# Performance work log

Hardware: AMD Instinct MI355X
Metric: run time of the kernel (lower is better)

The kernel has to match this reference:

```python
import jax, jax.numpy as jnp
import numpy as np

D_K = 64

def setup_inputs() -> dict:
    key = jax.random.key(0)
    kx, kq, kk, kv = jax.random.split(key, 4)
    B, T, D = 4, 2048, 1024
    s = 1.0 / np.sqrt(D)
    return {
        "x": jax.random.normal(kx, (B, T, D), dtype=jnp.float32),
        "Wq": jax.random.normal(kq, (D, D_K), dtype=jnp.float32) * s,
        "Wk": jax.random.normal(kk, (D, D_K), dtype=jnp.float32) * s,
        "Wv": jax.random.normal(kv, (D, D_K), dtype=jnp.float32) * s,
    }

def reference(x, Wq, Wk, Wv):
    # x: [B, T, D]; Wq/Wk/Wv: [D, d_k]
    Q = x @ Wq  # [B, T, d_k]
    K = x @ Wk
    V = x @ Wv
    scale = 1.0 / jnp.sqrt(jnp.asarray(Q.shape[-1], Q.dtype))
    scores = jnp.einsum('btd,bsd->bts', Q, K) * scale  # [B, T, T]
    T = scores.shape[-1]
    causal = jnp.tril(jnp.ones((T, T), dtype=bool))  # keep lower-tri incl diag
    masked = jnp.where(causal, scores, -jnp.inf)
    attn = jax.nn.softmax(masked, axis=-1)  # dropout p=0.0 -> identity
    context = jnp.einsum('bts,bsd->btd', attn, V)  # [B, T, d_k]
    return context
```

## Files before the change

### kernel.cpp

```cpp
#include <hip/hip_runtime.h>
#include <math.h>

#define BT    8192
#define TSEQ  2048
#define DIN   1024
#define DK    64

typedef __attribute__((ext_vector_type(8))) short bf16x8;
typedef __attribute__((ext_vector_type(4))) short bf16x4;
typedef __attribute__((ext_vector_type(4))) float f32x4;

static __device__ inline unsigned short f2bf(float f) {
    union { float f; unsigned u; } v; v.f = f;
    unsigned r = v.u + 0x7fff + ((v.u >> 16) & 1);
    return (unsigned short)(r >> 16);
}

static __device__ inline bf16x4 cvt4(float4 a) {
    bf16x4 r;
    r[0] = (short)f2bf(a.x); r[1] = (short)f2bf(a.y);
    r[2] = (short)f2bf(a.z); r[3] = (short)f2bf(a.w);
    return r;
}

__global__ __launch_bounds__(256) void wt_kernel(
    const float* __restrict__ Wq, const float* __restrict__ Wk,
    const float* __restrict__ Wv, unsigned short* __restrict__ WT)
{
    __shared__ float ws[64][65];
    const int tid = threadIdx.x;
    const int mat = blockIdx.x >> 4;
    const int k0  = (blockIdx.x & 15) << 6;
    const float* W = (mat == 0) ? Wq : ((mat == 1) ? Wk : Wv);

    const int j = tid & 63;
    for (int i = tid >> 6; i < 64; i += 4)
        ws[i][j] = W[(size_t)(k0 + i) * DK + j];
    __syncthreads();

    const int n  = tid & 63;
    const int c0 = (tid >> 6) << 4;
    unsigned short* dst = WT + (size_t)(mat * 64 + n) * DIN + k0 + c0;
    #pragma unroll
    for (int c = 0; c < 16; ++c) dst[c] = f2bf(ws[c0 + c][n]);
}

__global__ __launch_bounds__(256, 2) void proj_kernel(
    const float* __restrict__ x, const unsigned short* __restrict__ WT,
    unsigned short* __restrict__ Qb, unsigned short* __restrict__ Kb,
    unsigned short* __restrict__ VT)
{
    __shared__ unsigned short xs[16][1032];
    __shared__ unsigned short wtb[192][72];
    const int tid = threadIdx.x;
    const int m0 = blockIdx.x * 16;

    {
        const int r = tid >> 4;
        const int c = (tid & 15) << 2;
        const float* src = x + (size_t)(m0 + r) * DIN + c;
        float4 tmp[16];
        #pragma unroll
        for (int s = 0; s < 16; ++s) tmp[s] = *(const float4*)(src + s * 64);
        #pragma unroll
        for (int s = 0; s < 16; ++s) *(bf16x4*)&xs[r][c + s * 64] = cvt4(tmp[s]);
    }

    const int lane = tid & 63;
    const int w    = tid >> 6;
    const int lr = lane & 15, lg = lane >> 4;

    f32x4 acc[3];
    #pragma unroll
    for (int nt = 0; nt < 3; ++nt) acc[nt] = (f32x4){0.f, 0.f, 0.f, 0.f};

    const unsigned short* wt_w = WT + (size_t)w * 48 * DIN;
    bf16x8 cur[6], nxt[6];
    #pragma unroll
    for (int i = 0; i < 6; ++i) {
        const int c = lane + i * 64;
        const int nl = c >> 3;
        const int sl = c & 7;
        cur[i] = *(const bf16x8*)(wt_w + (size_t)nl * DIN + (sl << 3));
    }

    __syncthreads();

    for (int kc = 0; kc < 16; ++kc) {
        const int k0 = kc << 6;

        if (kc + 1 < 16) {
            #pragma unroll
            for (int i = 0; i < 6; ++i) {
                const int c = lane + i * 64;
                const int nl = c >> 3;
                const int sl = c & 7;
                nxt[i] = *(const bf16x8*)(wt_w + (size_t)nl * DIN
                                          + (k0 + 64) + (sl << 3));
            }
        }

        #pragma unroll
        for (int i = 0; i < 6; ++i) {
            const int c = lane + i * 64;
            const int n = w * 48 + (c >> 3);
            const int sl = c & 7;
            *(bf16x8*)&wtb[n][((sl + n) & 7) << 3] = cur[i];
        }
        asm volatile("s_waitcnt lgkmcnt(0)" ::: "memory");

        #pragma unroll
        for (int st = 0; st < 2; ++st) {
            const bf16x8 af = *(const bf16x8*)&xs[lr][k0 + (st << 5) + (lg << 3)];
            #pragma unroll
            for (int nt = 0; nt < 3; ++nt) {
                const int n = w * 48 + nt * 16 + lr;
                const int sl = (st << 2) + lg;
                const bf16x8 bf = *(const bf16x8*)&wtb[n][((sl + n) & 7) << 3];
                acc[nt] = __builtin_amdgcn_mfma_f32_16x16x32_bf16(af, bf, acc[nt], 0, 0, 0);
            }
        }

        if (kc + 1 < 16) {
            #pragma unroll
            for (int i = 0; i < 6; ++i) cur[i] = nxt[i];
        }
    }

    const float qsc = 0.125f * 1.44269504088896340736f;
    #pragma unroll
    for (int nt = 0; nt < 3; ++nt) {
        const int gct = w * 3 + nt;
        if (gct < 8) {
            #pragma unroll
            for (int r = 0; r < 4; ++r) {
                const int row = m0 + (lg << 2) + r;
                const float vv = acc[nt][r];
                if (gct < 4) Qb[(size_t)row * DK + gct * 16 + lr] = f2bf(vv * qsc);
                else         Kb[(size_t)row * DK + (gct - 4) * 16 + lr] = f2bf(vv);
            }
        } else {
            const int d = (gct - 8) * 16 + lr;
            const int t = m0 + (lg << 2);
            const int tb = t & (TSEQ - 1);
            const size_t tile = (size_t)(t >> 11) * 32 + (tb >> 6);
            ushort4 pk;
            pk.x = f2bf(acc[nt][0]); pk.y = f2bf(acc[nt][1]);
            pk.z = f2bf(acc[nt][2]); pk.w = f2bf(acc[nt][3]);
            *(ushort4*)&VT[(tile * DK + d) * 64 + (tb & 63)] = pk;
        }
    }
}

__global__ __launch_bounds__(256, 2) void attn_kernel(
    const unsigned short* __restrict__ Qb, const unsigned short* __restrict__ Kb,
    const unsigned short* __restrict__ VT, float* __restrict__ O)
{
    __shared__ __align__(16) unsigned short P_lds[4][16][72];
    __shared__ float Opart[4][16][68];
    __shared__ float mpart[4][16];
    __shared__ float Lpart[4][16];

    const int lane = threadIdx.x & 63;
    const int w    = threadIdx.x >> 6;
    const int i    = blockIdx.x;
    const int half = i >> 8;
    const int k    = i & 255;
    const int batch = k & 3;
    const int j    = k >> 2;
    const int qt_local = half ? j : (127 - j);
    const int q0 = (batch << 11) + (qt_local << 4);
    const int t0 = qt_local << 4;
    const int b  = batch;
    const int lr = lane & 15;
    const int lg = lane >> 4;

    const unsigned short* Qrow = Qb + (size_t)(q0 + lr) * DK + (lg << 3);
    const bf16x8 qf0 = *(const bf16x8*)(Qrow);
    const bf16x8 qf1 = *(const bf16x8*)(Qrow + 32);

    const unsigned short* Kbase = Kb + (size_t)b * TSEQ * DK;
    const unsigned short* Vbase = VT + (size_t)b * 32 * DK * 64;

    f32x4 oacc[4];
    #pragma unroll
    for (int dt = 0; dt < 4; ++dt) oacc[dt] = (f32x4){0.f, 0.f, 0.f, 0.f};
    float m[4] = {-INFINITY, -INFINITY, -INFINITY, -INFINITY};
    float L[4] = {0.f, 0.f, 0.f, 0.f};

    const int nkb = (t0 >> 6) + 1;

    bf16x8 kf0[4], kf1[4];
    if (w < nkb) {
        const int s0 = w << 6;
        #pragma unroll
        for (int ct = 0; ct < 4; ++ct) {
            const unsigned short* Krow =
                Kbase + (size_t)(s0 + ct * 16 + lr) * DK + (lg << 3);
            kf0[ct] = *(const bf16x8*)(Krow);
            kf1[ct] = *(const bf16x8*)(Krow + 32);
        }
    }

    for (int kb = w; kb < nkb; kb += 4) {
        const int s0 = kb << 6;

        f32x4 s[4];
        #pragma unroll
        for (int ct = 0; ct < 4; ++ct) {
            f32x4 a = (f32x4){0.f, 0.f, 0.f, 0.f};
            a = __builtin_amdgcn_mfma_f32_16x16x32_bf16(qf0, kf0[ct], a, 0, 0, 0);
            a = __builtin_amdgcn_mfma_f32_16x16x32_bf16(qf1, kf1[ct], a, 0, 0, 0);
            s[ct] = a;
        }

        bf16x8 vf0[4], vf1[4];
        {
            const unsigned short* Vtile = Vbase + (size_t)kb * DK * 64;
            #pragma unroll
            for (int dt = 0; dt < 4; ++dt) {
                const unsigned short* Vrow = Vtile + (dt * 16 + lr) * 64 + (lg << 3);
                vf0[dt] = *(const bf16x8*)(Vrow);
                vf1[dt] = *(const bf16x8*)(Vrow + 32);
            }
        }

        bf16x8 nk0[4], nk1[4];
        if (kb + 4 < nkb) {
            const int sn = (kb + 4) << 6;
            #pragma unroll
            for (int ct = 0; ct < 4; ++ct) {
                const unsigned short* Krow =
                    Kbase + (size_t)(sn + ct * 16 + lr) * DK + (lg << 3);
                nk0[ct] = *(const bf16x8*)(Krow);
                nk1[ct] = *(const bf16x8*)(Krow + 32);
            }
        }

        if (kb == nkb - 1) {
            #pragma unroll
            for (int ct = 0; ct < 4; ++ct)
                #pragma unroll
                for (int r = 0; r < 4; ++r)
                    if (s0 + ct * 16 + lr > t0 + lg * 4 + r) s[ct][r] = -INFINITY;
        }

        float pm[4];
        #pragma unroll
        for (int r = 0; r < 4; ++r)
            pm[r] = fmaxf(fmaxf(s[0][r], s[1][r]), fmaxf(s[2][r], s[3][r]));

        bool near = true;
        #pragma unroll
        for (int r = 0; r < 4; ++r)
            near = near && (pm[r] - m[r] <= 8.0f);

        if (!__all(near)) {
            float tmax[4];
            #pragma unroll
            for (int r = 0; r < 4; ++r) tmax[r] = pm[r];
            #pragma unroll
            for (int off = 1; off < 16; off <<= 1)
                #pragma unroll
                for (int r = 0; r < 4; ++r)
                    tmax[r] = fmaxf(tmax[r], __shfl_xor(tmax[r], off));

            float f[4];
            #pragma unroll
            for (int r = 0; r < 4; ++r) {
                const float mn = fmaxf(m[r], tmax[r]);
                f[r] = exp2f(m[r] - mn);
                m[r] = mn;
            }
            #pragma unroll
            for (int r = 0; r < 4; ++r) L[r] *= f[r];
            #pragma unroll
            for (int r = 0; r < 4; ++r) {
                oacc[0][r] *= f[r]; oacc[1][r] *= f[r];
                oacc[2][r] *= f[r]; oacc[3][r] *= f[r];
            }
        }

        float ps[4] = {0.f, 0.f, 0.f, 0.f};
        unsigned short pb[4][4];
        #pragma unroll
        for (int ct = 0; ct < 4; ++ct)
            #pragma unroll
            for (int r = 0; r < 4; ++r) {
                const float p = exp2f(s[ct][r] - m[r]);
                ps[r] += p;
                pb[ct][r] = f2bf(p);
            }
        #pragma unroll
        for (int r = 0; r < 4; ++r) L[r] += ps[r];

        #pragma unroll
        for (int ct = 0; ct < 4; ++ct)
            #pragma unroll
            for (int r = 0; r < 4; ++r)
                P_lds[w][lg * 4 + r][ct * 16 + lr] = pb[ct][r];
        asm volatile("s_waitcnt lgkmcnt(0)" ::: "memory");
        const bf16x8 pf0 = *(const bf16x8*)&P_lds[w][lr][(lg << 3)];
        const bf16x8 pf1 = *(const bf16x8*)&P_lds[w][lr][32 + (lg << 3)];

        #pragma unroll
        for (int dt = 0; dt < 4; ++dt) {
            oacc[dt] = __builtin_amdgcn_mfma_f32_16x16x32_bf16(pf0, vf0[dt], oacc[dt], 0, 0, 0);
            oacc[dt] = __builtin_amdgcn_mfma_f32_16x16x32_bf16(pf1, vf1[dt], oacc[dt], 0, 0, 0);
        }

        #pragma unroll
        for (int ct = 0; ct < 4; ++ct) { kf0[ct] = nk0[ct]; kf1[ct] = nk1[ct]; }
    }

    #pragma unroll
    for (int off = 1; off < 16; off <<= 1)
        #pragma unroll
        for (int r = 0; r < 4; ++r) L[r] += __shfl_xor(L[r], off);

    #pragma unroll
    for (int dt = 0; dt < 4; ++dt)
        #pragma unroll
        for (int r = 0; r < 4; ++r)
            Opart[w][(lg << 2) + r][dt * 16 + lr] = oacc[dt][r];
    if (lr == 0) {
        #pragma unroll
        for (int r = 0; r < 4; ++r) {
            mpart[w][(lg << 2) + r] = m[r];
            Lpart[w][(lg << 2) + r] = L[r];
        }
    }
    __syncthreads();

    #pragma unroll
    for (int r = 0; r < 4; ++r) {
        const int row = (lg << 2) + r;
        const float M = fmaxf(fmaxf(mpart[0][row], mpart[1][row]),
                              fmaxf(mpart[2][row], mpart[3][row]));
        float Lf = 0.f, o = 0.f;
        #pragma unroll
        for (int v = 0; v < 4; ++v) {
            const float fv = exp2f(mpart[v][row] - M);
            Lf += fv * Lpart[v][row];
            o  += fv * Opart[v][row][(w << 4) + lr];
        }
        O[(size_t)(q0 + row) * DK + (w << 4) + lr] = o / Lf;
    }
}

extern "C" void kernel_launch(void* const* d_in, const int* in_sizes, int n_in,
                              void* d_out, int out_size, void* d_ws, size_t ws_size,
                              hipStream_t stream) {
    const float* x  = (const float*)d_in[0];
    const float* Wq = (const float*)d_in[1];
    const float* Wk = (const float*)d_in[2];
    const float* Wv = (const float*)d_in[3];
    float* O = (float*)d_out;

    unsigned short* Qb = (unsigned short*)d_ws;
    unsigned short* Kb = Qb + (size_t)BT * DK;
    unsigned short* VT = Kb + (size_t)BT * DK;
    unsigned short* WT = VT + (size_t)BT * DK;

    wt_kernel  <<<dim3(48),  dim3(256), 0, stream>>>(Wq, Wk, Wv, WT);
    proj_kernel<<<dim3(512), dim3(256), 0, stream>>>(x, WT, Qb, Kb, VT);
    attn_kernel<<<dim3(512), dim3(256), 0, stream>>>(Qb, Kb, VT, O);
}
```

Before: 42.08 us.

## Process two query tiles per block with eight waves sharing K/V loads

The attention kernel now handles two adjacent 16-row query tiles per block. Each K/V tile loaded from global memory feeds the MFMAs for both query tiles, and eight waves split the key range instead of four. The grid drops to 256 blocks of 512 threads, and the software prefetch of the next K tile is removed. The cost is higher register pressure, a larger two-pass LDS reduction with an extra barrier, fewer blocks to balance the causal workload, and loss of K-load latency hiding.

```diff
diff --git a/kernel.cpp b/kernel.cpp
--- a/kernel.cpp
+++ b/kernel.cpp
@@ -152,47 +152,54 @@
     }
 }
 
-__global__ __launch_bounds__(256, 2) void attn_kernel(
+__global__ __launch_bounds__(512, 2) void attn_kernel(
     const unsigned short* __restrict__ Qb, const unsigned short* __restrict__ Kb,
     const unsigned short* __restrict__ VT, float* __restrict__ O)
 {
-    __shared__ __align__(16) unsigned short P_lds[4][16][72];
-    __shared__ float Opart[4][16][68];
-    __shared__ float mpart[4][16];
-    __shared__ float Lpart[4][16];
+    __shared__ __align__(16) unsigned short P_lds[8][16][72];
+    __shared__ float Opart[8][16][68];
+    __shared__ float mpart[8][16];
+    __shared__ float Lpart[8][16];
 
     const int lane = threadIdx.x & 63;
     const int w    = threadIdx.x >> 6;
     const int i    = blockIdx.x;
-    const int half = i >> 8;
-    const int k    = i & 255;
-    const int batch = k & 3;
-    const int j    = k >> 2;
-    const int qt_local = half ? j : (127 - j);
-    const int q0 = (batch << 11) + (qt_local << 4);
-    const int t0 = qt_local << 4;
-    const int b  = batch;
+    const int batch = i & 3;
+    const int jj   = 63 - (i >> 2);
+    const int t0A  = jj << 5;
+    const int t0B  = t0A + 16;
+    const int q0A  = (batch << 11) + t0A;
+    const int q0B  = q0A + 16;
     const int lr = lane & 15;
     const int lg = lane >> 4;
 
-    const unsigned short* Qrow = Qb + (size_t)(q0 + lr) * DK + (lg << 3);
-    const bf16x8 qf0 = *(const bf16x8*)(Qrow);
-    const bf16x8 qf1 = *(const bf16x8*)(Qrow + 32);
-
-    const unsigned short* Kbase = Kb + (size_t)b * TSEQ * DK;
-    const unsigned short* Vbase = VT + (size_t)b * 32 * DK * 64;
-
-    f32x4 oacc[4];
-    #pragma unroll
-    for (int dt = 0; dt < 4; ++dt) oacc[dt] = (f32x4){0.f, 0.f, 0.f, 0.f};
-    float m[4] = {-INFINITY, -INFINITY, -INFINITY, -INFINITY};
-    float L[4] = {0.f, 0.f, 0.f, 0.f};
-
-    const int nkb = (t0 >> 6) + 1;
-
-    bf16x8 kf0[4], kf1[4];
-    if (w < nkb) {
-        const int s0 = w << 6;
+    const unsigned short* QrowA = Qb + (size_t)(q0A + lr) * DK + (lg << 3);
+    const bf16x8 qfA0 = *(const bf16x8*)(QrowA);
+    const bf16x8 qfA1 = *(const bf16x8*)(QrowA + 32);
+    const unsigned short* QrowB = Qb + (size_t)(q0B + lr) * DK + (lg << 3);
+    const bf16x8 qfB0 = *(const bf16x8*)(QrowB);
+    const bf16x8 qfB1 = *(const bf16x8*)(QrowB + 32);
+
+    const unsigned short* Kbase = Kb + (size_t)batch * TSEQ * DK;
+    const unsigned short* Vbase = VT + (size_t)batch * 32 * DK * 64;
+
+    f32x4 oaccA[4], oaccB[4];
+    #pragma unroll
+    for (int dt = 0; dt < 4; ++dt) {
+        oaccA[dt] = (f32x4){0.f, 0.f, 0.f, 0.f};
+        oaccB[dt] = (f32x4){0.f, 0.f, 0.f, 0.f};
+    }
+    float mA[4] = {-INFINITY, -INFINITY, -INFINITY, -INFINITY};
+    float mB[4] = {-INFINITY, -INFINITY, -INFINITY, -INFINITY};
+    float LA[4] = {0.f, 0.f, 0.f, 0.f};
+    float LB[4] = {0.f, 0.f, 0.f, 0.f};
+
+    const int nkb = (t0B >> 6) + 1;
+
+    for (int kb = w; kb < nkb; kb += 8) {
+        const int s0 = kb << 6;
+
+        bf16x8 kf0[4], kf1[4], vf0[4], vf1[4];
         #pragma unroll
         for (int ct = 0; ct < 4; ++ct) {
             const unsigned short* Krow =
@@ -200,21 +207,6 @@
             kf0[ct] = *(const bf16x8*)(Krow);
             kf1[ct] = *(const bf16x8*)(Krow + 32);
         }
-    }
-
-    for (int kb = w; kb < nkb; kb += 4) {
-        const int s0 = kb << 6;
-
-        f32x4 s[4];
-        #pragma unroll
-        for (int ct = 0; ct < 4; ++ct) {
-            f32x4 a = (f32x4){0.f, 0.f, 0.f, 0.f};
-            a = __builtin_amdgcn_mfma_f32_16x16x32_bf16(qf0, kf0[ct], a, 0, 0, 0);
-            a = __builtin_amdgcn_mfma_f32_16x16x32_bf16(qf1, kf1[ct], a, 0, 0, 0);
-            s[ct] = a;
-        }
-
-        bf16x8 vf0[4], vf1[4];
         {
             const unsigned short* Vtile = Vbase + (size_t)kb * DK * 64;
             #pragma unroll
@@ -225,126 +217,210 @@
             }
         }
 
-        bf16x8 nk0[4], nk1[4];
-        if (kb + 4 < nkb) {
-            const int sn = (kb + 4) << 6;
-            #pragma unroll
-            for (int ct = 0; ct < 4; ++ct) {
-                const unsigned short* Krow =
-                    Kbase + (size_t)(sn + ct * 16 + lr) * DK + (lg << 3);
-                nk0[ct] = *(const bf16x8*)(Krow);
-                nk1[ct] = *(const bf16x8*)(Krow + 32);
-            }
+        f32x4 sA[4], sB[4];
+        #pragma unroll
+        for (int ct = 0; ct < 4; ++ct) {
+            f32x4 a = (f32x4){0.f, 0.f, 0.f, 0.f};
+            a = __builtin_amdgcn_mfma_f32_16x16x32_bf16(qfA0, kf0[ct], a, 0, 0, 0);
+            a = __builtin_amdgcn_mfma_f32_16x16x32_bf16(qfA1, kf1[ct], a, 0, 0, 0);
+            sA[ct] = a;
+            f32x4 b2 = (f32x4){0.f, 0.f, 0.f, 0.f};
+            b2 = __builtin_amdgcn_mfma_f32_16x16x32_bf16(qfB0, kf0[ct], b2, 0, 0, 0);
+            b2 = __builtin_amdgcn_mfma_f32_16x16x32_bf16(qfB1, kf1[ct], b2, 0, 0, 0);
+            sB[ct] = b2;
         }
 
         if (kb == nkb - 1) {
             #pragma unroll
             for (int ct = 0; ct < 4; ++ct)
                 #pragma unroll
+                for (int r = 0; r < 4; ++r) {
+                    const int key = s0 + ct * 16 + lr;
+                    if (key > t0A + lg * 4 + r) sA[ct][r] = -INFINITY;
+                    if (key > t0B + lg * 4 + r) sB[ct][r] = -INFINITY;
+                }
+        }
+
+        {
+            float pm[4];
+            #pragma unroll
+            for (int r = 0; r < 4; ++r)
+                pm[r] = fmaxf(fmaxf(sA[0][r], sA[1][r]), fmaxf(sA[2][r], sA[3][r]));
+            bool near = true;
+            #pragma unroll
+            for (int r = 0; r < 4; ++r) near = near && (pm[r] - mA[r] <= 8.0f);
+            if (!__all(near)) {
+                float tmax[4];
+                #pragma unroll
+                for (int r = 0; r < 4; ++r) tmax[r] = pm[r];
+                #pragma unroll
+                for (int off = 1; off < 16; off <<= 1)
+                    #pragma unroll
+                    for (int r = 0; r < 4; ++r)
+                        tmax[r] = fmaxf(tmax[r], __shfl_xor(tmax[r], off));
+                #pragma unroll
+                for (int r = 0; r < 4; ++r) {
+                    const float mn = fmaxf(mA[r], tmax[r]);
+                    const float f = exp2f(mA[r] - mn);
+                    mA[r] = mn; LA[r] *= f;
+                    oaccA[0][r] *= f; oaccA[1][r] *= f;
+                    oaccA[2][r] *= f; oaccA[3][r] *= f;
+                }
+            }
+            float ps[4] = {0.f, 0.f, 0.f, 0.f};
+            unsigned short pb[4][4];
+            #pragma unroll
+            for (int ct = 0; ct < 4; ++ct)
+                #pragma unroll
+                for (int r = 0; r < 4; ++r) {
+                    const float p = exp2f(sA[ct][r] - mA[r]);
+                    ps[r] += p;
+                    pb[ct][r] = f2bf(p);
+                }
+            #pragma unroll
+            for (int r = 0; r < 4; ++r) LA[r] += ps[r];
+            #pragma unroll
+            for (int ct = 0; ct < 4; ++ct)
+                #pragma unroll
                 for (int r = 0; r < 4; ++r)
-                    if (s0 + ct * 16 + lr > t0 + lg * 4 + r) s[ct][r] = -INFINITY;
-        }
-
-        float pm[4];
+                    P_lds[w][lg * 4 + r][ct * 16 + lr] = pb[ct][r];
+            asm volatile("s_waitcnt lgkmcnt(0)" ::: "memory");
+            const bf16x8 pf0 = *(const bf16x8*)&P_lds[w][lr][(lg << 3)];
+            const bf16x8 pf1 = *(const bf16x8*)&P_lds[w][lr][32 + (lg << 3)];
+            #pragma unroll
+            for (int dt = 0; dt < 4; ++dt) {
+                oaccA[dt] = __builtin_amdgcn_mfma_f32_16x16x32_bf16(pf0, vf0[dt], oaccA[dt], 0, 0, 0);
+                oaccA[dt] = __builtin_amdgcn_mfma_f32_16x16x32_bf16(pf1, vf1[dt], oaccA[dt], 0, 0, 0);
+            }
+        }
+
+        {
+            float pm[4];
+            #pragma unroll
+            for (int r = 0; r < 4; ++r)
+                pm[r] = fmaxf(fmaxf(sB[0][r], sB[1][r]), fmaxf(sB[2][r], sB[3][r]));
+            bool near = true;
+            #pragma unroll
+            for (int r = 0; r < 4; ++r) near = near && (pm[r] - mB[r] <= 8.0f);
+            if (!__all(near)) {
+                float tmax[4];
+                #pragma unroll
+                for (int r = 0; r < 4; ++r) tmax[r] = pm[r];
+                #pragma unroll
+                for (int off = 1; off < 16; off <<= 1)
+                    #pragma unroll
+                    for (int r = 0; r < 4; ++r)
+                        tmax[r] = fmaxf(tmax[r], __shfl_xor(tmax[r], off));
+                #pragma unroll
+                for (int r = 0; r < 4; ++r) {
+                    const float mn = fmaxf(mB[r], tmax[r]);
+                    const float f = exp2f(mB[r] - mn);
+                    mB[r] = mn; LB[r] *= f;
+                    oaccB[0][r] *= f; oaccB[1][r] *= f;
+                    oaccB[2][r] *= f; oaccB[3][r] *= f;
+                }
+            }
+            float ps[4] = {0.f, 0.f, 0.f, 0.f};
+            unsigned short pb[4][4];
+            #pragma unroll
+            for (int ct = 0; ct < 4; ++ct)
+                #pragma unroll
+                for (int r = 0; r < 4; ++r) {
+                    const float p = exp2f(sB[ct][r] - mB[r]);
+                    ps[r] += p;
+                    pb[ct][r] = f2bf(p);
+                }
+            #pragma unroll
+            for (int r = 0; r < 4; ++r) LB[r] += ps[r];
+            #pragma unroll
+            for (int ct = 0; ct < 4; ++ct)
+                #pragma unroll
+                for (int r = 0; r < 4; ++r)
+                    P_lds[w][lg * 4 + r][ct * 16 + lr] = pb[ct][r];
+            asm volatile("s_waitcnt lgkmcnt(0)" ::: "memory");
+            const bf16x8 pf0 = *(const bf16x8*)&P_lds[w][lr][(lg << 3)];
+            const bf16x8 pf1 = *(const bf16x8*)&P_lds[w][lr][32 + (lg << 3)];
+            #pragma unroll
+            for (int dt = 0; dt < 4; ++dt) {
+                oaccB[dt] = __builtin_amdgcn_mfma_f32_16x16x32_bf16(pf0, vf0[dt], oaccB[dt], 0, 0, 0);
+                oaccB[dt] = __builtin_amdgcn_mfma_f32_16x16x32_bf16(pf1, vf1[dt], oaccB[dt], 0, 0, 0);
+            }
+        }
+    }
+
+    #pragma unroll
+    for (int off = 1; off < 16; off <<= 1)
+        #pragma unroll
+        for (int r = 0; r < 4; ++r) {
+            LA[r] += __shfl_xor(LA[r], off);
+            LB[r] += __shfl_xor(LB[r], off);
+        }
+
+    #pragma unroll
+    for (int dt = 0; dt < 4; ++dt)
         #pragma unroll
         for (int r = 0; r < 4; ++r)
-            pm[r] = fmaxf(fmaxf(s[0][r], s[1][r]), fmaxf(s[2][r], s[3][r]));
-
-        bool near = true;
+            Opart[w][(lg << 2) + r][dt * 16 + lr] = oaccA[dt][r];
+    if (lr == 0) {
+        #pragma unroll
+        for (int r = 0; r < 4; ++r) {
+            mpart[w][(lg << 2) + r] = mA[r];
+            Lpart[w][(lg << 2) + r] = LA[r];
+        }
+    }
+    __syncthreads();
+    {
+        const int hhalf = w >> 2;
+        const int c     = w & 3;
+        #pragma unroll
+        for (int r = 0; r < 2; ++r) {
+            const int row = hhalf * 8 + (lg << 1) + r;
+            float M = -INFINITY;
+            #pragma unroll
+            for (int v = 0; v < 8; ++v) M = fmaxf(M, mpart[v][row]);
+            float Lf = 0.f, o = 0.f;
+            #pragma unroll
+            for (int v = 0; v < 8; ++v) {
+                const float fv = exp2f(mpart[v][row] - M);
+                Lf += fv * Lpart[v][row];
+                o  += fv * Opart[v][row][(c << 4) + lr];
+            }
+            O[(size_t)(q0A + row) * DK + (c << 4) + lr] = o / Lf;
+        }
+    }
+    __syncthreads();
+
+    #pragma unroll
+    for (int dt = 0; dt < 4; ++dt)
         #pragma unroll
         for (int r = 0; r < 4; ++r)
-            near = near && (pm[r] - m[r] <= 8.0f);
-
-        if (!__all(near)) {
-            float tmax[4];
-            #pragma unroll
-            for (int r = 0; r < 4; ++r) tmax[r] = pm[r];
-            #pragma unroll
-            for (int off = 1; off < 16; off <<= 1)
-                #pragma unroll
-                for (int r = 0; r < 4; ++r)
-                    tmax[r] = fmaxf(tmax[r], __shfl_xor(tmax[r], off));
-
-            float f[4];
-            #pragma unroll
-            for (int r = 0; r < 4; ++r) {
-                const float mn = fmaxf(m[r], tmax[r]);
-                f[r] = exp2f(m[r] - mn);
-                m[r] = mn;
-            }
-            #pragma unroll
-            for (int r = 0; r < 4; ++r) L[r] *= f[r];
-            #pragma unroll
-            for (int r = 0; r < 4; ++r) {
-                oacc[0][r] *= f[r]; oacc[1][r] *= f[r];
-                oacc[2][r] *= f[r]; oacc[3][r] *= f[r];
-            }
-        }
-
-        float ps[4] = {0.f, 0.f, 0.f, 0.f};
-        unsigned short pb[4][4];
-        #pragma unroll
-        for (int ct = 0; ct < 4; ++ct)
-            #pragma unroll
-            for (int r = 0; r < 4; ++r) {
-                const float p = exp2f(s[ct][r] - m[r]);
-                ps[r] += p;
-                pb[ct][r] = f2bf(p);
-            }
-        #pragma unroll
-        for (int r = 0; r < 4; ++r) L[r] += ps[r];
-
-        #pragma unroll
-        for (int ct = 0; ct < 4; ++ct)
-            #pragma unroll
-            for (int r = 0; r < 4; ++r)
-                P_lds[w][lg * 4 + r][ct * 16 + lr] = pb[ct][r];
-        asm volatile("s_waitcnt lgkmcnt(0)" ::: "memory");
-        const bf16x8 pf0 = *(const bf16x8*)&P_lds[w][lr][(lg << 3)];
-        const bf16x8 pf1 = *(const bf16x8*)&P_lds[w][lr][32 + (lg << 3)];
-
-        #pragma unroll
-        for (int dt = 0; dt < 4; ++dt) {
-            oacc[dt] = __builtin_amdgcn_mfma_f32_16x16x32_bf16(pf0, vf0[dt], oacc[dt], 0, 0, 0);
-            oacc[dt] = __builtin_amdgcn_mfma_f32_16x16x32_bf16(pf1, vf1[dt], oacc[dt], 0, 0, 0);
-        }
-
-        #pragma unroll
-        for (int ct = 0; ct < 4; ++ct) { kf0[ct] = nk0[ct]; kf1[ct] = nk1[ct]; }
-    }
-
-    #pragma unroll
-    for (int off = 1; off < 16; off <<= 1)
-        #pragma unroll
-        for (int r = 0; r < 4; ++r) L[r] += __shfl_xor(L[r], off);
-
-    #pragma unroll
-    for (int dt = 0; dt < 4; ++dt)
-        #pragma unroll
-        for (int r = 0; r < 4; ++r)
-            Opart[w][(lg << 2) + r][dt * 16 + lr] = oacc[dt][r];
+            Opart[w][(lg << 2) + r][dt * 16 + lr] = oaccB[dt][r];
     if (lr == 0) {
         #pragma unroll
         for (int r = 0; r < 4; ++r) {
-            mpart[w][(lg << 2) + r] = m[r];
-            Lpart[w][(lg << 2) + r] = L[r];
+            mpart[w][(lg << 2) + r] = mB[r];
+            Lpart[w][(lg << 2) + r] = LB[r];
         }
     }
     __syncthreads();
-
-    #pragma unroll
-    for (int r = 0; r < 4; ++r) {
-        const int row = (lg << 2) + r;
-        const float M = fmaxf(fmaxf(mpart[0][row], mpart[1][row]),
-                              fmaxf(mpart[2][row], mpart[3][row]));
-        float Lf = 0.f, o = 0.f;
-        #pragma unroll
-        for (int v = 0; v < 4; ++v) {
-            const float fv = exp2f(mpart[v][row] - M);
-            Lf += fv * Lpart[v][row];
-            o  += fv * Opart[v][row][(w << 4) + lr];
-        }
-        O[(size_t)(q0 + row) * DK + (w << 4) + lr] = o / Lf;
+    {
+        const int hhalf = w >> 2;
+        const int c     = w & 3;
+        #pragma unroll
+        for (int r = 0; r < 2; ++r) {
+            const int row = hhalf * 8 + (lg << 1) + r;
+            float M = -INFINITY;
+            #pragma unroll
+            for (int v = 0; v < 8; ++v) M = fmaxf(M, mpart[v][row]);
+            float Lf = 0.f, o = 0.f;
+            #pragma unroll
+            for (int v = 0; v < 8; ++v) {
+                const float fv = exp2f(mpart[v][row] - M);
+                Lf += fv * Lpart[v][row];
+                o  += fv * Opart[v][row][(c << 4) + lr];
+            }
+            O[(size_t)(q0B + row) * DK + (c << 4) + lr] = o / Lf;
+        }
     }
 }
 
@@ -364,5 +440,5 @@
 
     wt_kernel  <<<dim3(48),  dim3(256), 0, stream>>>(Wq, Wk, Wv, WT);
     proj_kernel<<<dim3(512), dim3(256), 0, stream>>>(x, WT, Qb, Kb, VT);
-    attn_kernel<<<dim3(512), dim3(256), 0, stream>>>(Qb, Kb, VT, O);
-}
+    attn_kernel<<<dim3(256), dim3(512), 0, stream>>>(Qb, Kb, VT, O);
+}
```

Result: slower. 44.08 us (+4.7%).
